# Optimization experiments

Hardware: AMD Instinct MI355X
Metric: run time of the kernel (lower is better)

The kernel has to match this reference:

```python
import jax, jax.numpy as jnp
import numpy as np

D_DIM = 100000  # vocabulary size
W_DIM = 128     # embedding width
BATCH = 4096    # number of (center, context) index pairs


def setup_inputs() -> dict:
    key = jax.random.key(0)
    k1, k2, kw1, kb1, kw2, kb2 = jax.random.split(key, 6)
    idx1 = jax.random.randint(k1, (BATCH,), 0, D_DIM, dtype=jnp.int64 if jax.config.jax_enable_x64 else jnp.int32)
    idx2 = jax.random.randint(k2, (BATCH,), 0, D_DIM, dtype=jnp.int64 if jax.config.jax_enable_x64 else jnp.int32)
    # torch.nn.Linear(D, W): weight [W, D], bias [W], uniform(-1/sqrt(D), 1/sqrt(D))
    bound = 1.0 / np.sqrt(D_DIM)
    W1 = jax.random.uniform(kw1, (W_DIM, D_DIM), jnp.float32, -bound, bound)
    b1 = jax.random.uniform(kb1, (W_DIM,), jnp.float32, -bound, bound)
    W2 = jax.random.uniform(kw2, (W_DIM, D_DIM), jnp.float32, -bound, bound)
    b2 = jax.random.uniform(kb2, (W_DIM,), jnp.float32, -bound, bound)
    return {"idx1": idx1, "idx2": idx2, "W1": W1, "b1": b1, "W2": W2, "b2": b2}


def reference(idx1, idx2, W1, b1, W2, b2):
    # Linear(one_hot(idx)) == weight[:, idx] + bias  -> direct row (column) gather.
    p1 = W1[:, idx1].T + b1              # [B, W_dim]
    p2 = W2[:, idx2].T + b2              # [B, W_dim]
    s = jax.nn.sigmoid(jnp.sum(p1 * p2, axis=-1))  # [B]
    # original: cat([1 - sigmoid, sigmoid]) -> [B, 2]
    return jnp.stack([1.0 - s, s], axis=-1)
```

## Files before the change

kernel.cpp:

```cpp
#include <hip/hip_runtime.h>
#include <math.h>

#define D_DIM 100000
#define W_DIM 128
#define BATCH 4096
#define BPAD  7168

__global__ __launch_bounds__(1024) void bucket_sort(
    const int* __restrict__ idx1, const int* __restrict__ idx2,
    int* __restrict__ sidx, int* __restrict__ inv)
{
    __shared__ int cnt[BPAD];
    __shared__ int ranks[BATCH];
    __shared__ int wsum[16];

    const int m = blockIdx.x;
    const int* __restrict__ idx = m ? idx2 : idx1;
    const int t    = threadIdx.x;
    const int lane = t & 63;
    const int wv   = t >> 6;

    for (int i = t; i < BPAD; i += 1024) cnt[i] = 0;
    __syncthreads();

    #pragma unroll
    for (int j = 0; j < 4; ++j) {
        const int i = t + j * 1024;
        ranks[i] = atomicAdd(&cnt[idx[i] >> 4], 1);
    }
    __syncthreads();

    const int base = t * 7;
    int c[7]; int s = 0;
    #pragma unroll
    for (int j = 0; j < 7; ++j) { c[j] = cnt[base + j]; s += c[j]; }

    int inc = s;
    #pragma unroll
    for (int off = 1; off < 64; off <<= 1) {
        const int v = __shfl_up(inc, off, 64);
        if (lane >= off) inc += v;
    }
    if (lane == 63) wsum[wv] = inc;
    __syncthreads();

    if (t < 16) {
        const int v = wsum[t];
        int winc = v;
        #pragma unroll
        for (int off = 1; off < 16; off <<= 1) {
            const int u = __shfl_up(winc, off, 16);
            if (t >= off) winc += u;
        }
        wsum[t] = winc - v;
    }
    __syncthreads();

    int excl = wsum[wv] + (inc - s);
    #pragma unroll
    for (int j = 0; j < 7; ++j) { cnt[base + j] = excl; excl += c[j]; }
    __syncthreads();

    #pragma unroll
    for (int j = 0; j < 4; ++j) {
        const int i = t + j * 1024;
        const int v = idx[i];
        const int pos = cnt[v >> 4] + ranks[i];
        sidx[(m << 12) + pos] = v;
        inv [(m << 12) + i]   = pos;
    }
}

__global__ __launch_bounds__(256) void gather(
    const int* __restrict__ sidx,
    const float* __restrict__ W1, const float* __restrict__ b1,
    const float* __restrict__ W2, const float* __restrict__ b2,
    float* __restrict__ Ps)
{
    const int g  = (blockIdx.x << 2) + (threadIdx.x >> 6);
    const int l  = threadIdx.x & 63;
    const int m  = g >> 12;
    const int rem = g & 4095;
    const int w   = rem >> 5;
    const int p0  = ((rem & 31) << 7) + (l << 1);

    const int2 ii = *(const int2*)&sidx[(m << 12) + p0];

    const float* __restrict__ row = (m ? W2 : W1) + (size_t)w * D_DIM;
    const float bias = m ? b2[w] : b1[w];

    const float v0 = row[ii.x] + bias;
    const float v1 = row[ii.y] + bias;

    float2* dst = (float2*)&Ps[(((size_t)(m << 7) + w) << 12) + p0];
    *dst = make_float2(v0, v1);
}

__global__ __launch_bounds__(256) void dot_sig(
    const float* __restrict__ Ps, const int* __restrict__ inv,
    float* __restrict__ out)
{
    __shared__ float red[4][64];
    const int wv = threadIdx.x >> 6;
    const int l  = threadIdx.x & 63;
    const int b  = (blockIdx.x << 6) + l;

    const int p1 = inv[b];
    const int p2 = inv[BATCH + b];
    const float* __restrict__ P1 = Ps;
    const float* __restrict__ P2 = Ps + ((size_t)W_DIM << 12);

    float acc = 0.0f;
    #pragma unroll
    for (int k = 0; k < 32; ++k) {
        const int w = (wv << 5) + k;
        acc += P1[((size_t)w << 12) + p1] * P2[((size_t)w << 12) + p2];
    }
    red[wv][l] = acc;
    __syncthreads();

    if (wv == 0) {
        const float v = red[0][l] + red[1][l] + red[2][l] + red[3][l];
        const float s = 1.0f / (1.0f + expf(-v));
        ((float2*)out)[b] = make_float2(1.0f - s, s);
    }
}

extern "C" void kernel_launch(void* const* d_in, const int* in_sizes, int n_in,
                              void* d_out, int out_size, void* d_ws, size_t ws_size,
                              hipStream_t stream)
{
    const int*   idx1 = (const int*)  d_in[0];
    const int*   idx2 = (const int*)  d_in[1];
    const float* W1   = (const float*)d_in[2];
    const float* b1   = (const float*)d_in[3];
    const float* W2   = (const float*)d_in[4];
    const float* b2   = (const float*)d_in[5];
    float* out = (float*)d_out;

    int* sidx = (int*)d_ws;
    int* inv  = sidx + 2 * BATCH;
    float* Ps = (float*)((char*)d_ws + 65536);

    bucket_sort<<<2, 1024, 0, stream>>>(idx1, idx2, sidx, inv);
    gather<<<2048, 256, 0, stream>>>(sidx, W1, b1, W2, b2, Ps);
    dot_sig<<<BATCH / 64, 256, 0, stream>>>(Ps, inv, out);
}
```

Before: 145.5 us.

## Coarsen gather per wave and split dot product across 16 lanes with shuffles

The gather kernel now gives each wave 8 iterations over a quarter of one weight row's sorted indices, which cuts the grid from 2048 to 256 blocks and improves per-row locality. The dot_sig kernel now assigns 16 lanes per batch element, each summing 8 of the 128 features, and reduces them with sub-wave shuffles instead of shared memory and __syncthreads. This raises thread count and parallelism in the dot product and removes the LDS reduction. In exchange, the gather has fewer blocks to hide the latency of its scattered loads, and lanes in dot_sig read scattered addresses.

```diff
diff --git a/kernel.cpp b/kernel.cpp
--- a/kernel.cpp
+++ b/kernel.cpp
@@ -77,33 +77,36 @@
     const float* __restrict__ W2, const float* __restrict__ b2,
     float* __restrict__ Ps)
 {
-    const int g  = (blockIdx.x << 2) + (threadIdx.x >> 6);
-    const int l  = threadIdx.x & 63;
-    const int m  = g >> 12;
-    const int rem = g & 4095;
-    const int w   = rem >> 5;
-    const int p0  = ((rem & 31) << 7) + (l << 1);
-
-    const int2 ii = *(const int2*)&sidx[(m << 12) + p0];
+    const int g = (blockIdx.x << 2) + (threadIdx.x >> 6);
+    const int l = threadIdx.x & 63;
+    const int m = g >> 9;
+    const int w = (g >> 2) & 127;
+    const int q = g & 3;
 
     const float* __restrict__ row = (m ? W2 : W1) + (size_t)w * D_DIM;
     const float bias = m ? b2[w] : b1[w];
 
-    const float v0 = row[ii.x] + bias;
-    const float v1 = row[ii.y] + bias;
+    const int pbase = (q << 10) + (l << 1);
+    const int* __restrict__ sp = sidx + (m << 12);
+    float* __restrict__ dst = Ps + (((size_t)(m << 7) + w) << 12);
 
-    float2* dst = (float2*)&Ps[(((size_t)(m << 7) + w) << 12) + p0];
-    *dst = make_float2(v0, v1);
+    #pragma unroll
+    for (int it = 0; it < 8; ++it) {
+        const int p = pbase + (it << 7);
+        const int2 ii = *(const int2*)&sp[p];
+        const float v0 = row[ii.x] + bias;
+        const float v1 = row[ii.y] + bias;
+        *(float2*)&dst[p] = make_float2(v0, v1);
+    }
 }
 
 __global__ __launch_bounds__(256) void dot_sig(
     const float* __restrict__ Ps, const int* __restrict__ inv,
     float* __restrict__ out)
 {
-    __shared__ float red[4][64];
-    const int wv = threadIdx.x >> 6;
-    const int l  = threadIdx.x & 63;
-    const int b  = (blockIdx.x << 6) + l;
+    const int t   = (blockIdx.x << 8) + threadIdx.x;
+    const int b   = t >> 4;
+    const int seg = t & 15;
 
     const int p1 = inv[b];
     const int p2 = inv[BATCH + b];
@@ -112,16 +115,17 @@
 
     float acc = 0.0f;
     #pragma unroll
-    for (int k = 0; k < 32; ++k) {
-        const int w = (wv << 5) + k;
+    for (int k = 0; k < 8; ++k) {
+        const int w = (seg << 3) + k;
         acc += P1[((size_t)w << 12) + p1] * P2[((size_t)w << 12) + p2];
     }
-    red[wv][l] = acc;
-    __syncthreads();
+    acc += __shfl_down(acc, 8, 16);
+    acc += __shfl_down(acc, 4, 16);
+    acc += __shfl_down(acc, 2, 16);
+    acc += __shfl_down(acc, 1, 16);
 
-    if (wv == 0) {
-        const float v = red[0][l] + red[1][l] + red[2][l] + red[3][l];
-        const float s = 1.0f / (1.0f + expf(-v));
+    if (seg == 0) {
+        const float s = 1.0f / (1.0f + expf(-acc));
         ((float2*)out)[b] = make_float2(1.0f - s, s);
     }
 }
@@ -143,6 +147,6 @@
     float* Ps = (float*)((char*)d_ws + 65536);
 
     bucket_sort<<<2, 1024, 0, stream>>>(idx1, idx2, sidx, inv);
-    gather<<<2048, 256, 0, stream>>>(sidx, W1, b1, W2, b2, Ps);
-    dot_sig<<<BATCH / 64, 256, 0, stream>>>(Ps, inv, out);
+    gather<<<256, 256, 0, stream>>>(sidx, W1, b1, W2, b2, Ps);
+    dot_sig<<<256, 256, 0, stream>>>(Ps, inv, out);
 }
```

Result: faster. 136.4 us (-6.3%).
